# Optimization experiments

Measured on AMD Instinct MI355X. Metric: run time of the kernel, lower is better.

Reference implementation:

```python
import jax, jax.numpy as jnp
import numpy as np

IN_C = 256
INTER_C = 128


def _conv1x1(x_flat, w, b):
    # x_flat: [n, c_in, N]; w: [c_out, c_in]; b: [c_out] -> [n, c_out, N]
    return jnp.einsum('oc,bcn->bon', w, x_flat) + b[None, :, None]


def setup_inputs() -> dict:
    key = jax.random.key(0)
    ks = jax.random.split(key, 9)
    x = jax.random.normal(ks[0], (4, IN_C, 64, 64), dtype=jnp.float32)
    s_in = 1.0 / np.sqrt(IN_C)
    s_mid = 1.0 / np.sqrt(INTER_C)
    return {
        'x': x,
        'g_w': jax.random.uniform(ks[1], (INTER_C, IN_C), jnp.float32, -s_in, s_in),
        'g_b': jax.random.uniform(ks[2], (INTER_C,), jnp.float32, -s_in, s_in),
        'theta_w': jax.random.uniform(ks[3], (INTER_C, IN_C), jnp.float32, -s_in, s_in),
        'theta_b': jax.random.uniform(ks[4], (INTER_C,), jnp.float32, -s_in, s_in),
        'phi_w': jax.random.uniform(ks[5], (INTER_C, IN_C), jnp.float32, -s_in, s_in),
        'phi_b': jax.random.uniform(ks[6], (INTER_C,), jnp.float32, -s_in, s_in),
        'out_w': jax.random.uniform(ks[7], (IN_C, INTER_C), jnp.float32, -s_mid, s_mid),
        'out_b': jax.random.uniform(ks[8], (IN_C,), jnp.float32, -s_mid, s_mid),
    }


def reference(x, g_w, g_b, theta_w, theta_b, phi_w, phi_b, out_w, out_b):
    n, c, h, w = x.shape
    N = h * w
    x_flat = x.reshape(n, c, N)
    # 1x1-conv projections
    g_x = _conv1x1(x_flat, g_w, g_b).transpose(0, 2, 1)       # [n, N, ci]
    theta_x = _conv1x1(x_flat, theta_w, theta_b).transpose(0, 2, 1)  # [n, N, ci]
    phi_x = _conv1x1(x_flat, phi_w, phi_b)                    # [n, ci, N]
    # dot_product variant: pairwise weight normalized by N (no softmax)
    pairwise_weight = jnp.matmul(theta_x, phi_x) / N          # [n, N, N]
    y = jnp.matmul(pairwise_weight, g_x)                      # [n, N, ci]
    y = y.transpose(0, 2, 1)                                  # [n, ci, N]
    out = x_flat + _conv1x1(y, out_w, out_b)                  # residual
    return out.reshape(n, c, h, w)
```

## Files before the change

kernel.cpp:

```cpp
#include <hip/hip_runtime.h>
#include <hip/hip_bf16.h>


#define CC   256
#define NSP  4096
#define NB   4
#define KSPLIT 16

typedef __attribute__((ext_vector_type(8))) short bf16x8;
typedef __attribute__((ext_vector_type(4))) float f32x4;

#define F_WEND 1048576
#define H_TT   0
#define H_PG   2097152
#define H_S2   6291456
#define H_WH   6356992
#define H_OWH  6455296
#define H_W2   6488064

__device__ __forceinline__ unsigned short f2bf(float f) {
  __hip_bfloat16 h = __float2bfloat16(f);
  return __builtin_bit_cast(unsigned short, h);
}
__device__ __forceinline__ uint4 pack8(const unsigned short* h) {
  uint4 u;
  u.x = (unsigned)h[0] | ((unsigned)h[1] << 16);
  u.y = (unsigned)h[2] | ((unsigned)h[3] << 16);
  u.z = (unsigned)h[4] | ((unsigned)h[5] << 16);
  u.w = (unsigned)h[6] | ((unsigned)h[7] << 16);
  return u;
}

__device__ __forceinline__ void wave_gemm_bt(const unsigned short* __restrict__ A, int pitchA,
                                             const unsigned short* __restrict__ B, int pitchB,
                                             int K, int lane, f32x4 acc[4][4]) {
  int lm = lane & 15, lq = lane >> 4;
  const unsigned short* ap[4];
  const unsigned short* bp[4];
#pragma unroll
  for (int i = 0; i < 4; ++i) {
    ap[i] = A + (size_t)(i * 16 + lm) * pitchA + lq * 8;
    bp[i] = B + (size_t)(i * 16 + lm) * pitchB + lq * 8;
  }
  bf16x8 a0[4], b0[4];
#pragma unroll
  for (int i = 0; i < 4; ++i) {
    a0[i] = *(const bf16x8*)(ap[i]);
    b0[i] = *(const bf16x8*)(bp[i]);
  }
  for (int k = 32; k < K; k += 32) {
    bf16x8 a1[4], b1[4];
#pragma unroll
    for (int i = 0; i < 4; ++i) {
      a1[i] = *(const bf16x8*)(ap[i] + k);
      b1[i] = *(const bf16x8*)(bp[i] + k);
    }
#pragma unroll
    for (int mi = 0; mi < 4; ++mi)
#pragma unroll
      for (int ni = 0; ni < 4; ++ni)
        acc[mi][ni] = __builtin_amdgcn_mfma_f32_16x16x32_bf16(a0[mi], b0[ni], acc[mi][ni], 0, 0, 0);
#pragma unroll
    for (int i = 0; i < 4; ++i) { a0[i] = a1[i]; b0[i] = b1[i]; }
  }
#pragma unroll
  for (int mi = 0; mi < 4; ++mi)
#pragma unroll
    for (int ni = 0; ni < 4; ++ni)
      acc[mi][ni] = __builtin_amdgcn_mfma_f32_16x16x32_bf16(a0[mi], b0[ni], acc[mi][ni], 0, 0, 0);
}

__global__ __launch_bounds__(256) void kW(const float* __restrict__ g_w,
                                          const float* __restrict__ theta_w,
                                          const float* __restrict__ phi_w,
                                          const float* __restrict__ out_w,
                                          unsigned short* __restrict__ wsh) {
  int idx = (blockIdx.x * 256 + threadIdx.x) * 4;
  const float* src;
  unsigned short* dst;
  if (idx < 98304) {
    int r = idx >> 8;
    src = (r < 128) ? (g_w + idx)
        : (r < 256) ? (theta_w + idx - 32768)
                    : (phi_w + idx - 65536);
    dst = wsh + H_WH + idx;
  } else {
    src = out_w + (idx - 98304);
    dst = wsh + H_OWH + (idx - 98304);
  }
  float4 v = *(const float4*)src;
  uint2 o;
  o.x = (unsigned)f2bf(v.x) | ((unsigned)f2bf(v.y) << 16);
  o.y = (unsigned)f2bf(v.z) | ((unsigned)f2bf(v.w) << 16);
  *(uint2*)dst = o;
}

__global__ __launch_bounds__(256) void kP(
    const float* __restrict__ g_b, const float* __restrict__ theta_b,
    const float* __restrict__ phi_b, const float* __restrict__ x,
    unsigned short* __restrict__ wsh) {
  __shared__ float T[64][33];
  __shared__ unsigned short XL[32 * 256];
  __shared__ float biasL[384];
  int bid = blockIdx.x;
  int b = bid >> 7, c = bid & 127;
  int t = threadIdx.x;
  if (t < 128) {
    biasL[t]       = g_b[t];
    biasL[128 + t] = theta_b[t];
    biasL[256 + t] = phi_b[t];
  }
  for (int s = 0; s < 4; ++s) {
    int r = t >> 2, j = t & 3;
    const float* xr = x + ((size_t)b * CC + s * 64 + r) * NSP + c * 32 + j * 8;
    float4 f0 = *(const float4*)(xr);
    float4 f1 = *(const float4*)(xr + 4);
    T[r][j * 8 + 0] = f0.x; T[r][j * 8 + 1] = f0.y;
    T[r][j * 8 + 2] = f0.z; T[r][j * 8 + 3] = f0.w;
    T[r][j * 8 + 4] = f1.x; T[r][j * 8 + 5] = f1.y;
    T[r][j * 8 + 6] = f1.z; T[r][j * 8 + 7] = f1.w;
    __syncthreads();
    int nr = t >> 3, j2 = t & 7;
    unsigned short o[8];
#pragma unroll
    for (int i = 0; i < 8; ++i) o[i] = f2bf(T[j2 * 8 + i][nr]);
    int kidx = s * 64 + j2 * 8;
    int sw = (nr & 7) << 3;
    *(uint4*)(XL + ((nr * 256 + kidx) ^ sw)) = pack8(o);
    __syncthreads();
  }

  int w = t >> 6, lane = t & 63;
  int lm = lane & 15, lq = lane >> 4;
  int bsw = (lm & 7) << 3;
  const unsigned short* aw[2];
  int bidx[2];
#pragma unroll
  for (int i = 0; i < 2; ++i)
    aw[i] = wsh + H_WH + (size_t)(w * 32 + i * 16 + lm) * 256 + lq * 8;
#pragma unroll
  for (int j = 0; j < 2; ++j)
    bidx[j] = (j * 16 + lm) * 256 + lq * 8;

  f32x4 ag[2][2] = {}, at2[2][2] = {}, ap2[2][2] = {};
#pragma unroll 2
  for (int k = 0; k < 256; k += 32) {
    bf16x8 bb[2], xg[2], xt[2], xp[2];
#pragma unroll
    for (int j = 0; j < 2; ++j) bb[j] = *(const bf16x8*)(XL + ((bidx[j] + k) ^ bsw));
#pragma unroll
    for (int i = 0; i < 2; ++i) {
      xg[i] = *(const bf16x8*)(aw[i] + k);
      xt[i] = *(const bf16x8*)(aw[i] + 32768 + k);
      xp[i] = *(const bf16x8*)(aw[i] + 65536 + k);
    }
#pragma unroll
    for (int mi = 0; mi < 2; ++mi)
#pragma unroll
      for (int ni = 0; ni < 2; ++ni) {
        ag[mi][ni]  = __builtin_amdgcn_mfma_f32_16x16x32_bf16(xg[mi], bb[ni], ag[mi][ni], 0, 0, 0);
        at2[mi][ni] = __builtin_amdgcn_mfma_f32_16x16x32_bf16(xt[mi], bb[ni], at2[mi][ni], 0, 0, 0);
        ap2[mi][ni] = __builtin_amdgcn_mfma_f32_16x16x32_bf16(xp[mi], bb[ni], ap2[mi][ni], 0, 0, 0);
      }
  }

  size_t tb = (size_t)b * 524288;
#pragma unroll
  for (int mi = 0; mi < 2; ++mi) {
    int p0 = w * 32 + mi * 16 + lq * 4;
#pragma unroll
    for (int ni = 0; ni < 2; ++ni) {
      int n = c * 32 + ni * 16 + lm;
      unsigned short u0 = f2bf(at2[mi][ni][0] + biasL[128 + p0 + 0]);
      unsigned short u1 = f2bf(at2[mi][ni][1] + biasL[128 + p0 + 1]);
      unsigned short u2 = f2bf(at2[mi][ni][2] + biasL[128 + p0 + 2]);
      unsigned short u3 = f2bf(at2[mi][ni][3] + biasL[128 + p0 + 3]);
      uint2 o;
      o.x = (unsigned)u0 | ((unsigned)u1 << 16);
      o.y = (unsigned)u2 | ((unsigned)u3 << 16);
      *(uint2*)(wsh + H_TT + tb + (size_t)n * 128 + p0) = o;
    }
  }

  __syncthreads();
#pragma unroll
  for (int mi = 0; mi < 2; ++mi)
#pragma unroll
    for (int ni = 0; ni < 2; ++ni) {
      int nl = ni * 16 + lm;
#pragma unroll
      for (int rr = 0; rr < 4; ++rr) {
        int p = w * 32 + mi * 16 + lq * 4 + rr;
        XL[p * 32 + nl]         = f2bf(ag[mi][ni][rr] + biasL[p]);
        XL[(128 + p) * 32 + nl] = f2bf(ap2[mi][ni][rr] + biasL[256 + p]);
      }
    }
  __syncthreads();
  size_t pbo = (size_t)b * 1048576;
#pragma unroll
  for (int r4 = 0; r4 < 4; ++r4) {
    int row = r4 * 64 + (t >> 2);
    int coff = (t & 3) * 8;
    *(uint4*)(wsh + H_PG + pbo + (size_t)row * NSP + c * 32 + coff) =
        *(uint4*)(XL + row * 32 + coff);
  }
}

__global__ __launch_bounds__(256) void kS(const unsigned short* __restrict__ wsh,
                                          float* __restrict__ wsf) {
  int bid = blockIdx.x;
  int b = bid >> 4, ks = bid & 15;
  int t = threadIdx.x, w = t >> 6, lane = t & 63;
  int lm = lane & 15, lq = lane >> 4;
  int qm = w >> 1, qn = w & 1;
  const unsigned short* A = wsh + H_PG + (size_t)b * 1048576 +
                            (size_t)(128 + qm * 64) * NSP + ks * 256;
  const unsigned short* B = wsh + H_PG + (size_t)b * 1048576 +
                            (size_t)(qn * 64) * NSP + ks * 256;
  f32x4 acc[4][4] = {};
  wave_gemm_bt(A, NSP, B, NSP, 256, lane, acc);
  float* P = wsf + (size_t)(b * KSPLIT + ks) * 16384;
#pragma unroll
  for (int mi = 0; mi < 4; ++mi)
#pragma unroll
    for (int rr = 0; rr < 4; ++rr) {
      int p = qm * 64 + mi * 16 + lq * 4 + rr;
#pragma unroll
      for (int ni = 0; ni < 4; ++ni)
        P[p * 128 + qn * 64 + ni * 16 + lm] = acc[mi][ni][rr];
    }
}

__global__ __launch_bounds__(256) void kR(const float* __restrict__ wsf,
                                          unsigned short* __restrict__ wsh) {
  int bid = blockIdx.x;
  int b = bid >> 4, e = bid & 15;
  int t = threadIdx.x;
  int base = e * 1024 + t * 4;
  const float* PB = wsf + (size_t)b * KSPLIT * 16384;
  float4 s = {0.f, 0.f, 0.f, 0.f};
#pragma unroll
  for (int ks = 0; ks < KSPLIT; ++ks) {
    float4 p = *(const float4*)(PB + (size_t)ks * 16384 + base);
    s.x += p.x; s.y += p.y; s.z += p.z; s.w += p.w;
  }
  uint2 o;
  o.x = (unsigned)f2bf(s.x) | ((unsigned)f2bf(s.y) << 16);
  o.y = (unsigned)f2bf(s.z) | ((unsigned)f2bf(s.w) << 16);
  *(uint2*)(wsh + H_S2 + (size_t)b * 16384 + base) = o;
}

__global__ __launch_bounds__(256) void kW2(unsigned short* __restrict__ wsh) {
  int bid = blockIdx.x;
  int b = bid >> 2, is = bid & 3;
  int t = threadIdx.x, w = t >> 6, lane = t & 63;
  int lm = lane & 15, lq = lane >> 4;
  const unsigned short* A = wsh + H_OWH + (size_t)(is * 64) * 128;
  const unsigned short* B = wsh + H_S2 + (size_t)b * 16384 + (size_t)(w * 32) * 128;
  f32x4 acc[4][2] = {};
  for (int k = 0; k < 128; k += 32) {
    bf16x8 a[4], bb[2];
#pragma unroll
    for (int i = 0; i < 4; ++i)
      a[i] = *(const bf16x8*)(A + (size_t)(i * 16 + lm) * 128 + lq * 8 + k);
#pragma unroll
    for (int j = 0; j < 2; ++j)
      bb[j] = *(const bf16x8*)(B + (size_t)(j * 16 + lm) * 128 + lq * 8 + k);
#pragma unroll
    for (int mi = 0; mi < 4; ++mi)
#pragma unroll
      for (int ni = 0; ni < 2; ++ni)
        acc[mi][ni] = __builtin_amdgcn_mfma_f32_16x16x32_bf16(a[mi], bb[ni], acc[mi][ni], 0, 0, 0);
  }
  const float inv = 1.0f / 4096.0f;
#pragma unroll
  for (int mi = 0; mi < 4; ++mi)
#pragma unroll
    for (int rr = 0; rr < 4; ++rr) {
      int i = is * 64 + mi * 16 + lq * 4 + rr;
#pragma unroll
      for (int ni = 0; ni < 2; ++ni) {
        int p = w * 32 + ni * 16 + lm;
        wsh[H_W2 + (size_t)b * 32768 + (size_t)i * 128 + p] = f2bf(acc[mi][ni][rr] * inv);
      }
    }
}

__global__ __launch_bounds__(256) void kD(const unsigned short* __restrict__ wsh,
                                          const float* __restrict__ x,
                                          const float* __restrict__ out_b,
                                          float* __restrict__ out) {
  int bid = blockIdx.x;
  int b = bid >> 7, r7 = bid & 127;
  int tm = r7 >> 6, tn = r7 & 63;
  int t = threadIdx.x, w = t >> 6, lane = t & 63;
  int wm = w >> 1, wn = w & 1;
  int lm = lane & 15, lq = lane >> 4;
  int rb = tm * 128 + wm * 64, cb = tn * 64 + wn * 32;
  const unsigned short* A = wsh + H_W2 + (size_t)b * 32768;
  const unsigned short* B = wsh + H_TT + (size_t)b * 524288;
  const unsigned short* ap[4];
  const unsigned short* bp[2];
#pragma unroll
  for (int i = 0; i < 4; ++i)
    ap[i] = A + (size_t)(rb + i * 16 + lm) * 128 + lq * 8;
#pragma unroll
  for (int j = 0; j < 2; ++j)
    bp[j] = B + (size_t)(cb + j * 16 + lm) * 128 + lq * 8;

  f32x4 acc[4][2] = {};
  bf16x8 a0[4], b0[2];
#pragma unroll
  for (int i = 0; i < 4; ++i) a0[i] = *(const bf16x8*)(ap[i]);
#pragma unroll
  for (int j = 0; j < 2; ++j) b0[j] = *(const bf16x8*)(bp[j]);
  for (int k = 32; k < 128; k += 32) {
    bf16x8 a1[4], b1[2];
#pragma unroll
    for (int i = 0; i < 4; ++i) a1[i] = *(const bf16x8*)(ap[i] + k);
#pragma unroll
    for (int j = 0; j < 2; ++j) b1[j] = *(const bf16x8*)(bp[j] + k);
#pragma unroll
    for (int mi = 0; mi < 4; ++mi)
#pragma unroll
      for (int ni = 0; ni < 2; ++ni)
        acc[mi][ni] = __builtin_amdgcn_mfma_f32_16x16x32_bf16(a0[mi], b0[ni], acc[mi][ni], 0, 0, 0);
#pragma unroll
    for (int i = 0; i < 4; ++i) a0[i] = a1[i];
#pragma unroll
    for (int j = 0; j < 2; ++j) b0[j] = b1[j];
  }
#pragma unroll
  for (int mi = 0; mi < 4; ++mi)
#pragma unroll
    for (int ni = 0; ni < 2; ++ni)
      acc[mi][ni] = __builtin_amdgcn_mfma_f32_16x16x32_bf16(a0[mi], b0[ni], acc[mi][ni], 0, 0, 0);

#pragma unroll
  for (int mi = 0; mi < 4; ++mi)
#pragma unroll
    for (int rr = 0; rr < 4; ++rr) {
      int row = rb + mi * 16 + lq * 4 + rr;
      float bi = out_b[row];
#pragma unroll
      for (int ni = 0; ni < 2; ++ni) {
        int col = cb + ni * 16 + lm;
        size_t off = ((size_t)b * CC + row) * NSP + col;
        out[off] = acc[mi][ni][rr] + x[off] + bi;
      }
    }
}

extern "C" void kernel_launch(void* const* d_in, const int* in_sizes, int n_in,
                              void* d_out, int out_size, void* d_ws, size_t ws_size,
                              hipStream_t stream) {
  const float* x       = (const float*)d_in[0];
  const float* g_w     = (const float*)d_in[1];
  const float* g_b     = (const float*)d_in[2];
  const float* theta_w = (const float*)d_in[3];
  const float* theta_b = (const float*)d_in[4];
  const float* phi_w   = (const float*)d_in[5];
  const float* phi_b   = (const float*)d_in[6];
  const float* out_w   = (const float*)d_in[7];
  const float* out_b   = (const float*)d_in[8];
  float* wsf = (float*)d_ws;
  unsigned short* wsh = (unsigned short*)(wsf + F_WEND);
  float* out = (float*)d_out;

  kW<<<dim3(128), dim3(256), 0, stream>>>(g_w, theta_w, phi_w, out_w, wsh);
  kP<<<dim3(512), dim3(256), 0, stream>>>(g_b, theta_b, phi_b, x, wsh);
  kS<<<dim3(64), dim3(256), 0, stream>>>(wsh, wsf);
  kR<<<dim3(64), dim3(256), 0, stream>>>(wsf, wsh);
  kW2<<<dim3(16), dim3(256), 0, stream>>>(wsh);
  kD<<<dim3(512), dim3(256), 0, stream>>>(wsh, x, out_b, out);
}
```

Measured before the change: 125.8 us.

## Raise split-K and grid sizes, prefetch kP operands, fold out_w conversion into kW2

Doubles the split-K factor in the theta-phi Gram kernel (kS) to launch more blocks, and halves the kD output tile so that kernel launches twice as many blocks. kP's projection loop becomes an explicit register double-buffered prefetch. out_w is no longer converted to bf16 in kW; kW2 now loads and converts it from fp32 inline. The intent is better GPU occupancy across the small grids. The cost is a larger partial-sum workspace for the reduction kernel kR to read and more redundant loads in kD.

```diff
diff --git a/kernel.cpp b/kernel.cpp
--- a/kernel.cpp
+++ b/kernel.cpp
@@ -5,18 +5,17 @@
 #define CC   256
 #define NSP  4096
 #define NB   4
-#define KSPLIT 16
+#define KSPLIT 32
 
 typedef __attribute__((ext_vector_type(8))) short bf16x8;
 typedef __attribute__((ext_vector_type(4))) float f32x4;
 
-#define F_WEND 1048576
+#define F_WEND 2097152
 #define H_TT   0
 #define H_PG   2097152
 #define H_S2   6291456
 #define H_WH   6356992
-#define H_OWH  6455296
-#define H_W2   6488064
+#define H_W2   6455296
 
 __device__ __forceinline__ unsigned short f2bf(float f) {
   __hip_bfloat16 h = __float2bfloat16(f);
@@ -30,6 +29,16 @@
   u.w = (unsigned)h[6] | ((unsigned)h[7] << 16);
   return u;
 }
+__device__ __forceinline__ bf16x8 ld_cvt8(const float* __restrict__ p) {
+  float4 lo = *(const float4*)p;
+  float4 hi = *(const float4*)(p + 4);
+  bf16x8 r;
+  r[0] = (short)f2bf(lo.x); r[1] = (short)f2bf(lo.y);
+  r[2] = (short)f2bf(lo.z); r[3] = (short)f2bf(lo.w);
+  r[4] = (short)f2bf(hi.x); r[5] = (short)f2bf(hi.y);
+  r[6] = (short)f2bf(hi.z); r[7] = (short)f2bf(hi.w);
+  return r;
+}
 
 __device__ __forceinline__ void wave_gemm_bt(const unsigned short* __restrict__ A, int pitchA,
                                              const unsigned short* __restrict__ B, int pitchB,
@@ -73,26 +82,17 @@
 __global__ __launch_bounds__(256) void kW(const float* __restrict__ g_w,
                                           const float* __restrict__ theta_w,
                                           const float* __restrict__ phi_w,
-                                          const float* __restrict__ out_w,
                                           unsigned short* __restrict__ wsh) {
   int idx = (blockIdx.x * 256 + threadIdx.x) * 4;
-  const float* src;
-  unsigned short* dst;
-  if (idx < 98304) {
-    int r = idx >> 8;
-    src = (r < 128) ? (g_w + idx)
-        : (r < 256) ? (theta_w + idx - 32768)
-                    : (phi_w + idx - 65536);
-    dst = wsh + H_WH + idx;
-  } else {
-    src = out_w + (idx - 98304);
-    dst = wsh + H_OWH + (idx - 98304);
-  }
+  int r = idx >> 8;
+  const float* src = (r < 128) ? (g_w + idx)
+                   : (r < 256) ? (theta_w + idx - 32768)
+                               : (phi_w + idx - 65536);
   float4 v = *(const float4*)src;
   uint2 o;
   o.x = (unsigned)f2bf(v.x) | ((unsigned)f2bf(v.y) << 16);
   o.y = (unsigned)f2bf(v.z) | ((unsigned)f2bf(v.w) << 16);
-  *(uint2*)dst = o;
+  *(uint2*)(wsh + H_WH + idx) = o;
 }
 
 __global__ __launch_bounds__(256) void kP(
@@ -143,26 +143,46 @@
     bidx[j] = (j * 16 + lm) * 256 + lq * 8;
 
   f32x4 ag[2][2] = {}, at2[2][2] = {}, ap2[2][2] = {};
-#pragma unroll 2
-  for (int k = 0; k < 256; k += 32) {
-    bf16x8 bb[2], xg[2], xt[2], xp[2];
-#pragma unroll
-    for (int j = 0; j < 2; ++j) bb[j] = *(const bf16x8*)(XL + ((bidx[j] + k) ^ bsw));
+  bf16x8 bb0[2], xg0[2], xt0[2], xp0[2];
+#pragma unroll
+  for (int j = 0; j < 2; ++j) bb0[j] = *(const bf16x8*)(XL + (bidx[j] ^ bsw));
+#pragma unroll
+  for (int i = 0; i < 2; ++i) {
+    xg0[i] = *(const bf16x8*)(aw[i]);
+    xt0[i] = *(const bf16x8*)(aw[i] + 32768);
+    xp0[i] = *(const bf16x8*)(aw[i] + 65536);
+  }
+  for (int k = 32; k < 256; k += 32) {
+    bf16x8 bb1[2], xg1[2], xt1[2], xp1[2];
+#pragma unroll
+    for (int j = 0; j < 2; ++j) bb1[j] = *(const bf16x8*)(XL + ((bidx[j] + k) ^ bsw));
 #pragma unroll
     for (int i = 0; i < 2; ++i) {
-      xg[i] = *(const bf16x8*)(aw[i] + k);
-      xt[i] = *(const bf16x8*)(aw[i] + 32768 + k);
-      xp[i] = *(const bf16x8*)(aw[i] + 65536 + k);
+      xg1[i] = *(const bf16x8*)(aw[i] + k);
+      xt1[i] = *(const bf16x8*)(aw[i] + 32768 + k);
+      xp1[i] = *(const bf16x8*)(aw[i] + 65536 + k);
     }
 #pragma unroll
     for (int mi = 0; mi < 2; ++mi)
 #pragma unroll
       for (int ni = 0; ni < 2; ++ni) {
-        ag[mi][ni]  = __builtin_amdgcn_mfma_f32_16x16x32_bf16(xg[mi], bb[ni], ag[mi][ni], 0, 0, 0);
-        at2[mi][ni] = __builtin_amdgcn_mfma_f32_16x16x32_bf16(xt[mi], bb[ni], at2[mi][ni], 0, 0, 0);
-        ap2[mi][ni] = __builtin_amdgcn_mfma_f32_16x16x32_bf16(xp[mi], bb[ni], ap2[mi][ni], 0, 0, 0);
+        ag[mi][ni]  = __builtin_amdgcn_mfma_f32_16x16x32_bf16(xg0[mi], bb0[ni], ag[mi][ni], 0, 0, 0);
+        at2[mi][ni] = __builtin_amdgcn_mfma_f32_16x16x32_bf16(xt0[mi], bb0[ni], at2[mi][ni], 0, 0, 0);
+        ap2[mi][ni] = __builtin_amdgcn_mfma_f32_16x16x32_bf16(xp0[mi], bb0[ni], ap2[mi][ni], 0, 0, 0);
       }
-  }
+#pragma unroll
+    for (int i = 0; i < 2; ++i) {
+      bb0[i] = bb1[i]; xg0[i] = xg1[i]; xt0[i] = xt1[i]; xp0[i] = xp1[i];
+    }
+  }
+#pragma unroll
+  for (int mi = 0; mi < 2; ++mi)
+#pragma unroll
+    for (int ni = 0; ni < 2; ++ni) {
+      ag[mi][ni]  = __builtin_amdgcn_mfma_f32_16x16x32_bf16(xg0[mi], bb0[ni], ag[mi][ni], 0, 0, 0);
+      at2[mi][ni] = __builtin_amdgcn_mfma_f32_16x16x32_bf16(xt0[mi], bb0[ni], at2[mi][ni], 0, 0, 0);
+      ap2[mi][ni] = __builtin_amdgcn_mfma_f32_16x16x32_bf16(xp0[mi], bb0[ni], ap2[mi][ni], 0, 0, 0);
+    }
 
   size_t tb = (size_t)b * 524288;
 #pragma unroll
@@ -209,16 +229,16 @@
 __global__ __launch_bounds__(256) void kS(const unsigned short* __restrict__ wsh,
                                           float* __restrict__ wsf) {
   int bid = blockIdx.x;
-  int b = bid >> 4, ks = bid & 15;
+  int b = bid >> 5, ks = bid & 31;
   int t = threadIdx.x, w = t >> 6, lane = t & 63;
   int lm = lane & 15, lq = lane >> 4;
   int qm = w >> 1, qn = w & 1;
   const unsigned short* A = wsh + H_PG + (size_t)b * 1048576 +
-                            (size_t)(128 + qm * 64) * NSP + ks * 256;
+                            (size_t)(128 + qm * 64) * NSP + ks * 128;
   const unsigned short* B = wsh + H_PG + (size_t)b * 1048576 +
-                            (size_t)(qn * 64) * NSP + ks * 256;
+                            (size_t)(qn * 64) * NSP + ks * 128;
   f32x4 acc[4][4] = {};
-  wave_gemm_bt(A, NSP, B, NSP, 256, lane, acc);
+  wave_gemm_bt(A, NSP, B, NSP, 128, lane, acc);
   float* P = wsf + (size_t)(b * KSPLIT + ks) * 16384;
 #pragma unroll
   for (int mi = 0; mi < 4; ++mi)
@@ -250,19 +270,19 @@
   *(uint2*)(wsh + H_S2 + (size_t)b * 16384 + base) = o;
 }
 
-__global__ __launch_bounds__(256) void kW2(unsigned short* __restrict__ wsh) {
+__global__ __launch_bounds__(256) void kW2(unsigned short* __restrict__ wsh,
+                                           const float* __restrict__ out_w) {
   int bid = blockIdx.x;
   int b = bid >> 2, is = bid & 3;
   int t = threadIdx.x, w = t >> 6, lane = t & 63;
   int lm = lane & 15, lq = lane >> 4;
-  const unsigned short* A = wsh + H_OWH + (size_t)(is * 64) * 128;
   const unsigned short* B = wsh + H_S2 + (size_t)b * 16384 + (size_t)(w * 32) * 128;
   f32x4 acc[4][2] = {};
   for (int k = 0; k < 128; k += 32) {
     bf16x8 a[4], bb[2];
 #pragma unroll
     for (int i = 0; i < 4; ++i)
-      a[i] = *(const bf16x8*)(A + (size_t)(i * 16 + lm) * 128 + lq * 8 + k);
+      a[i] = ld_cvt8(out_w + (size_t)(is * 64 + i * 16 + lm) * 128 + lq * 8 + k);
 #pragma unroll
     for (int j = 0; j < 2; ++j)
       bb[j] = *(const bf16x8*)(B + (size_t)(j * 16 + lm) * 128 + lq * 8 + k);
@@ -291,53 +311,51 @@
                                           const float* __restrict__ out_b,
                                           float* __restrict__ out) {
   int bid = blockIdx.x;
-  int b = bid >> 7, r7 = bid & 127;
-  int tm = r7 >> 6, tn = r7 & 63;
+  int b = bid >> 8, r8 = bid & 255;
+  int rq = r8 >> 6, ct = r8 & 63;
   int t = threadIdx.x, w = t >> 6, lane = t & 63;
   int wm = w >> 1, wn = w & 1;
   int lm = lane & 15, lq = lane >> 4;
-  int rb = tm * 128 + wm * 64, cb = tn * 64 + wn * 32;
+  int rb = rq * 64 + wm * 32, cb = ct * 64 + wn * 32;
   const unsigned short* A = wsh + H_W2 + (size_t)b * 32768;
   const unsigned short* B = wsh + H_TT + (size_t)b * 524288;
-  const unsigned short* ap[4];
+  const unsigned short* ap[2];
   const unsigned short* bp[2];
 #pragma unroll
-  for (int i = 0; i < 4; ++i)
+  for (int i = 0; i < 2; ++i) {
     ap[i] = A + (size_t)(rb + i * 16 + lm) * 128 + lq * 8;
-#pragma unroll
-  for (int j = 0; j < 2; ++j)
-    bp[j] = B + (size_t)(cb + j * 16 + lm) * 128 + lq * 8;
-
-  f32x4 acc[4][2] = {};
-  bf16x8 a0[4], b0[2];
-#pragma unroll
-  for (int i = 0; i < 4; ++i) a0[i] = *(const bf16x8*)(ap[i]);
-#pragma unroll
-  for (int j = 0; j < 2; ++j) b0[j] = *(const bf16x8*)(bp[j]);
+    bp[i] = B + (size_t)(cb + i * 16 + lm) * 128 + lq * 8;
+  }
+  f32x4 acc[2][2] = {};
+  bf16x8 a0[2], b0[2];
+#pragma unroll
+  for (int i = 0; i < 2; ++i) {
+    a0[i] = *(const bf16x8*)(ap[i]);
+    b0[i] = *(const bf16x8*)(bp[i]);
+  }
   for (int k = 32; k < 128; k += 32) {
-    bf16x8 a1[4], b1[2];
-#pragma unroll
-    for (int i = 0; i < 4; ++i) a1[i] = *(const bf16x8*)(ap[i] + k);
-#pragma unroll
-    for (int j = 0; j < 2; ++j) b1[j] = *(const bf16x8*)(bp[j] + k);
-#pragma unroll
-    for (int mi = 0; mi < 4; ++mi)
+    bf16x8 a1[2], b1[2];
+#pragma unroll
+    for (int i = 0; i < 2; ++i) {
+      a1[i] = *(const bf16x8*)(ap[i] + k);
+      b1[i] = *(const bf16x8*)(bp[i] + k);
+    }
+#pragma unroll
+    for (int mi = 0; mi < 2; ++mi)
 #pragma unroll
       for (int ni = 0; ni < 2; ++ni)
         acc[mi][ni] = __builtin_amdgcn_mfma_f32_16x16x32_bf16(a0[mi], b0[ni], acc[mi][ni], 0, 0, 0);
 #pragma unroll
-    for (int i = 0; i < 4; ++i) a0[i] = a1[i];
-#pragma unroll
-    for (int j = 0; j < 2; ++j) b0[j] = b1[j];
-  }
-#pragma unroll
-  for (int mi = 0; mi < 4; ++mi)
+    for (int i = 0; i < 2; ++i) { a0[i] = a1[i]; b0[i] = b1[i]; }
+  }
+#pragma unroll
+  for (int mi = 0; mi < 2; ++mi)
 #pragma unroll
     for (int ni = 0; ni < 2; ++ni)
       acc[mi][ni] = __builtin_amdgcn_mfma_f32_16x16x32_bf16(a0[mi], b0[ni], acc[mi][ni], 0, 0, 0);
 
 #pragma unroll
-  for (int mi = 0; mi < 4; ++mi)
+  for (int mi = 0; mi < 2; ++mi)
 #pragma unroll
     for (int rr = 0; rr < 4; ++rr) {
       int row = rb + mi * 16 + lq * 4 + rr;
@@ -367,10 +385,10 @@
   unsigned short* wsh = (unsigned short*)(wsf + F_WEND);
   float* out = (float*)d_out;
 
-  kW<<<dim3(128), dim3(256), 0, stream>>>(g_w, theta_w, phi_w, out_w, wsh);
+  kW<<<dim3(96), dim3(256), 0, stream>>>(g_w, theta_w, phi_w, wsh);
   kP<<<dim3(512), dim3(256), 0, stream>>>(g_b, theta_b, phi_b, x, wsh);
-  kS<<<dim3(64), dim3(256), 0, stream>>>(wsh, wsf);
+  kS<<<dim3(128), dim3(256), 0, stream>>>(wsh, wsf);
   kR<<<dim3(64), dim3(256), 0, stream>>>(wsf, wsh);
-  kW2<<<dim3(16), dim3(256), 0, stream>>>(wsh);
-  kD<<<dim3(512), dim3(256), 0, stream>>>(wsh, x, out_b, out);
-}
+  kW2<<<dim3(16), dim3(256), 0, stream>>>(wsh, out_w);
+  kD<<<dim3(1024), dim3(256), 0, stream>>>(wsh, x, out_b, out);
+}
```

After: 126.5 us. About the same (+0.6%).
